# Performance work log

Measured on AMD Instinct MI355X. Metric: run time of the kernel, lower is better.

Reference implementation:

```python
import jax, jax.numpy as jnp
import numpy as np

B, S, A = 4096, 512, 64  # batch, state_dim, n_actions
H1, H2 = 1024, 512       # hidden_dims
EPS = 1e-8


def setup_inputs() -> dict:
    key = jax.random.key(0)
    ks = jax.random.split(key, 7)
    return {
        "states": jax.random.normal(ks[0], (B, S), dtype=jnp.float32),
        "W1": jax.random.normal(ks[1], (H1, S + A), dtype=jnp.float32) * 0.05,
        "b1": jax.random.normal(ks[2], (H1,), dtype=jnp.float32) * 0.01,
        "W2": jax.random.normal(ks[3], (H2, H1), dtype=jnp.float32) * 0.05,
        "b2": jax.random.normal(ks[4], (H2,), dtype=jnp.float32) * 0.01,
        "Wq": jax.random.normal(ks[5], (1, H2), dtype=jnp.float32) * 0.05,
        "bq": jax.random.normal(ks[6], (1,), dtype=jnp.float32) * 0.01,
    }


def _ff_layer(h, W, b):
    # L2-normalize over feature dim (torch dim=1 for 2D input), then linear + ReLU
    hn = h / (jnp.linalg.norm(h, axis=-1, keepdims=True) + EPS)
    return jax.nn.relu(jnp.einsum("abi,oi->abo", hn, W) + b)


def reference(states, W1, b1, W2, b2, Wq, bq):
    # Vectorized form of q_values: loop over actions becomes a leading axis a.
    # x_in[a, b] = concat(states[b], one_hot(a))  (overlay_type='standard')
    onehot = jnp.eye(A, dtype=states.dtype)                         # [A, A]
    x = jnp.concatenate(
        [jnp.broadcast_to(states[None], (A, B, S)),
         jnp.broadcast_to(onehot[:, None, :], (A, B, A))], axis=-1)  # [A, B, S+A]
    h = _ff_layer(x, W1, b1)   # [A, B, H1]
    h = _ff_layer(h, W2, b2)   # [A, B, H2]
    q = jnp.einsum("abh,oh->abo", h, Wq)[..., 0] + bq[0]            # [A, B]
    return q.T                                                       # [B, A]
```

## Files before the change

### kernel.cpp

```cpp
#include <hip/hip_runtime.h>
#include <stdint.h>

#define NB 4096
#define NS 512
#define NA 64
#define NH1 1024
#define NH2 512

typedef __attribute__((ext_vector_type(8))) short bf16x8;
typedef __attribute__((ext_vector_type(4))) float f32x4;

__device__ __forceinline__ unsigned short f2bf(float f) {
    union { float f; unsigned u; } v; v.f = f;
    return (unsigned short)((v.u + 0x8000u) >> 16);
}
__device__ __forceinline__ float bf2f(unsigned short h) {
    union { float f; unsigned u; } v; v.u = ((unsigned)h) << 16;
    return v.f;
}
__device__ __forceinline__ float bflo(unsigned u) {
    union { unsigned u; float f; } v; v.u = u << 16; return v.f;
}
__device__ __forceinline__ float bfhi(unsigned u) {
    union { unsigned u; float f; } v; v.u = u & 0xFFFF0000u; return v.f;
}
__device__ __forceinline__ unsigned packtrunc(float lo, float hi) {
    union { float f; unsigned u; } a, b; a.f = lo; b.f = hi;
    return __builtin_amdgcn_perm(b.u, a.u, 0x07060302u);
}
__device__ __forceinline__ void split2(float x, unsigned short& h, unsigned short& l) {
    unsigned short hh = f2bf(x);
    h = hh;
    l = f2bf(x - bf2f(hh));
}

__global__ void knorm(const float* __restrict__ S, float* __restrict__ nb) {
    int b = blockIdx.x; int l = threadIdx.x;
    const float* row = S + b * NS;
    float s = 0.f;
    for (int k = l; k < NS; k += 64) { float v = row[k]; s = fmaf(v, v, s); }
    for (int off = 32; off; off >>= 1) s += __shfl_down(s, off, 64);
    if (l == 0) nb[b] = sqrtf(s + 1.0f) + 1e-8f;
}

__global__ void kprep(const float* __restrict__ W1, const float* __restrict__ W2,
                      unsigned short* __restrict__ W2f, unsigned short* __restrict__ caT2) {
    int i = blockIdx.x * 256 + threadIdx.x;
    if (i < 524288) {
        int j = i & 7; int l = (i >> 3) & 63; int c = (i >> 9) & 31; int kc = i >> 14;
        int n = c * 16 + (l >> 2);
        int g = (l & 3) ^ ((n >> 1) & 3);
        int k = kc * 32 + g * 8 + j;
        W2f[i] = f2bf(W2[(size_t)n * NH1 + k]);
    } else {
        int j2 = i - 524288;
        int kk = j2 & 31; int a_loc = (j2 >> 5) & 15;
        int kc = (j2 >> 9) & 31; int att = j2 >> 14;
        int o = kc * 32 + kk;
        caT2[j2] = f2bf(W1[(size_t)o * 576 + 512 + att * 16 + a_loc]);
    }
}

__global__ __launch_bounds__(256) void kgemm1(
        const float* __restrict__ Sm, const float* __restrict__ W1,
        const float* __restrict__ b1, const float* __restrict__ nb,
        unsigned short* __restrict__ Gt) {
    const int m0 = (blockIdx.x >> 4) * 64;
    const int n0 = (blockIdx.x & 15) * 64;
    __shared__ unsigned short Ah[64][40], Al[64][40], Bh[64][40], Bl[64][40];
    int t = threadIdx.x;
    int lane = t & 63, wave = t >> 6;
    int wr = wave >> 1, wc = wave & 1;
    int qd = lane >> 4, cl = lane & 15;
    int r = t >> 2, seg = t & 3;
    f32x4 acc[2][2] = {};

    for (int k0 = 0; k0 < 512; k0 += 32) {
        {
            const float4* as4 = (const float4*)(Sm + (size_t)(m0 + r) * NS + k0 + seg * 8);
            const float4* bs4 = (const float4*)(W1 + (size_t)(n0 + r) * 576 + k0 + seg * 8);
            unsigned* ah = (unsigned*)&Ah[r][seg * 8];
            unsigned* al = (unsigned*)&Al[r][seg * 8];
            unsigned* bh = (unsigned*)&Bh[r][seg * 8];
            unsigned* bl = (unsigned*)&Bl[r][seg * 8];
#pragma unroll
            for (int v = 0; v < 2; v++) {
                float4 fa = as4[v];
                unsigned short h0,h1,h2,h3,l0,l1,l2,l3;
                split2(fa.x,h0,l0); split2(fa.y,h1,l1); split2(fa.z,h2,l2); split2(fa.w,h3,l3);
                ah[v*2]   = (unsigned)h0 | ((unsigned)h1 << 16);
                ah[v*2+1] = (unsigned)h2 | ((unsigned)h3 << 16);
                al[v*2]   = (unsigned)l0 | ((unsigned)l1 << 16);
                al[v*2+1] = (unsigned)l2 | ((unsigned)l3 << 16);
                float4 fb = bs4[v];
                split2(fb.x,h0,l0); split2(fb.y,h1,l1); split2(fb.z,h2,l2); split2(fb.w,h3,l3);
                bh[v*2]   = (unsigned)h0 | ((unsigned)h1 << 16);
                bh[v*2+1] = (unsigned)h2 | ((unsigned)h3 << 16);
                bl[v*2]   = (unsigned)l0 | ((unsigned)l1 << 16);
                bl[v*2+1] = (unsigned)l2 | ((unsigned)l3 << 16);
            }
        }
        __syncthreads();
        bf16x8 a_h[2], a_l[2], b_h[2], b_l[2];
#pragma unroll
        for (int mt = 0; mt < 2; mt++) {
            a_h[mt] = *(const bf16x8*)&Ah[wr*32 + mt*16 + cl][qd*8];
            a_l[mt] = *(const bf16x8*)&Al[wr*32 + mt*16 + cl][qd*8];
        }
#pragma unroll
        for (int nt = 0; nt < 2; nt++) {
            b_h[nt] = *(const bf16x8*)&Bh[wc*32 + nt*16 + cl][qd*8];
            b_l[nt] = *(const bf16x8*)&Bl[wc*32 + nt*16 + cl][qd*8];
        }
#pragma unroll
        for (int mt = 0; mt < 2; mt++)
#pragma unroll
            for (int nt = 0; nt < 2; nt++) {
                acc[mt][nt] = __builtin_amdgcn_mfma_f32_16x16x32_bf16(a_h[mt], b_h[nt], acc[mt][nt], 0, 0, 0);
                acc[mt][nt] = __builtin_amdgcn_mfma_f32_16x16x32_bf16(a_h[mt], b_l[nt], acc[mt][nt], 0, 0, 0);
                acc[mt][nt] = __builtin_amdgcn_mfma_f32_16x16x32_bf16(a_l[mt], b_h[nt], acc[mt][nt], 0, 0, 0);
            }
        __syncthreads();
    }
#pragma unroll
    for (int mt = 0; mt < 2; mt++)
#pragma unroll
        for (int i = 0; i < 4; i++) {
            int m = m0 + wr*32 + mt*16 + qd*4 + i;
            float nbv = nb[m];
#pragma unroll
            for (int nt = 0; nt < 2; nt++) {
                int n = n0 + wc*32 + nt*16 + cl;
                float val = fmaf(b1[n], nbv, acc[mt][nt][i]);
                Gt[((size_t)(n >> 5) * NB + m) * 32 + (n & 31)] = f2bf(val);
            }
        }
}

__global__ __launch_bounds__(256, 2) void kmain(
        const unsigned short* __restrict__ Gt,
        const unsigned short* __restrict__ caT2,
        const unsigned short* __restrict__ W2f,
        const float* __restrict__ nb,
        const float* __restrict__ b2, const float* __restrict__ Wq,
        const float* __restrict__ bq, float* __restrict__ out) {
    int bid = blockIdx.x;
    int at = bid & 3;
    int bt = bid >> 2;

    __shared__ __align__(16) unsigned short As[8][64][40];
    __shared__ float invnh[64];
    __shared__ float qred[64][4];

    int t = threadIdx.x;
    int lane = t & 63, wc = t >> 6;
    int l15 = lane & 15, l4 = lane >> 4;

    int row = t >> 2, kd = t & 3;
    int ab = row >> 2, bb = row & 3;
    const unsigned short* gG = Gt + ((size_t)(bt * 4 + bb)) * 32 + kd * 8;
    const unsigned short* gC = caT2 + (size_t)at * 16384 + ab * 32 + kd * 8;

    float sq = 0.f;
    f32x4 acc[4][8] = {};
    bf16x8 g_v, c_v;

    auto agen = [&](int slot) {
        const unsigned* gd = (const unsigned*)&g_v;
        const unsigned* cd = (const unsigned*)&c_v;
        unsigned ow[4];
#pragma unroll
        for (int p = 0; p < 4; p++) {
            float u0 = fmaxf(bflo(gd[p]) + bflo(cd[p]), 0.f);
            float u1 = fmaxf(bfhi(gd[p]) + bfhi(cd[p]), 0.f);
            sq = fmaf(u0, u0, sq);
            sq = fmaf(u1, u1, sq);
            ow[p] = packtrunc(u0, u1);
        }
        *(bf16x8*)&As[slot][row][kd * 8] = *(bf16x8*)ow;
    };

    const int boff = (wc * 128 + l15) * 32 + ((l4 ^ ((l15 >> 1) & 3)) << 3);
    const unsigned short* gB = W2f + boff;

    bf16x8 bfrL[4], bfrH[4];

    g_v = *(const bf16x8*)gG;
    c_v = *(const bf16x8*)gC;
#pragma unroll
    for (int p = 0; p < 4; ++p) {
        agen(p);
        gG += (size_t)NB * 32;
        gC += 512;
        g_v = *(const bf16x8*)gG;
        c_v = *(const bf16x8*)gC;
    }
#pragma unroll
    for (int j = 0; j < 4; j++)
        bfrL[j] = *(const bf16x8*)(gB + j * 512);
#pragma unroll
    for (int j = 0; j < 4; j++)
        bfrH[j] = *(const bf16x8*)(gB + (4 + j) * 512);
    gB += 16384;

    for (int it = 0; it < 32; ++it) {
        if ((it & 3) == 0) {
            asm volatile("s_waitcnt lgkmcnt(0)" ::: "memory");
            __builtin_amdgcn_s_barrier();
            __builtin_amdgcn_sched_barrier(0);
        }
        int rs = it & 7;

        bf16x8 af[4];
#pragma unroll
        for (int mt = 0; mt < 4; mt++)
            af[mt] = *(const bf16x8*)&As[rs][mt * 16 + l15][l4 * 8];

        if (it < 28) agen((it + 4) & 7);
        if (it < 27) {
            gG += (size_t)NB * 32;
            gC += 512;
            g_v = *(const bf16x8*)gG;
            c_v = *(const bf16x8*)gC;
        }

        __builtin_amdgcn_s_setprio(1);
#pragma unroll
        for (int nt = 0; nt < 4; nt++)
#pragma unroll
            for (int mt = 0; mt < 4; mt++)
                acc[mt][nt] = __builtin_amdgcn_mfma_f32_16x16x32_bf16(af[mt], bfrL[nt], acc[mt][nt], 0, 0, 0);
        __builtin_amdgcn_s_setprio(0);

        if (it < 31) {
#pragma unroll
            for (int j = 0; j < 4; j++)
                bfrL[j] = *(const bf16x8*)(gB + j * 512);
        }

        __builtin_amdgcn_s_setprio(1);
#pragma unroll
        for (int nt = 0; nt < 4; nt++)
#pragma unroll
            for (int mt = 0; mt < 4; mt++)
                acc[mt][4 + nt] = __builtin_amdgcn_mfma_f32_16x16x32_bf16(af[mt], bfrH[nt], acc[mt][4 + nt], 0, 0, 0);
        __builtin_amdgcn_s_setprio(0);

        if (it < 31) {
#pragma unroll
            for (int j = 0; j < 4; j++)
                bfrH[j] = *(const bf16x8*)(gB + (4 + j) * 512);
            gB += 16384;
        }
    }

    sq += __shfl_xor(sq, 1, 64);
    sq += __shfl_xor(sq, 2, 64);
    if (kd == 0) invnh[row] = 1.0f / (sqrtf(sq) + 1e-8f * nb[bt * 4 + bb]);
    __syncthreads();

    float wqv[8], b2v[8];
#pragma unroll
    for (int nt = 0; nt < 8; nt++) {
        int o = wc * 128 + nt * 16 + l15;
        wqv[nt] = Wq[o]; b2v[nt] = b2[o];
    }
#pragma unroll
    for (int mt = 0; mt < 4; mt++) {
#pragma unroll
        for (int i = 0; i < 4; i++) {
            int R = mt * 16 + l4 * 4 + i;
            float inv = invnh[R];
            float qp = 0.f;
#pragma unroll
            for (int nt = 0; nt < 8; nt++) {
                float z = fmaf(acc[mt][nt][i], inv, b2v[nt]);
                z = fmaxf(z, 0.f);
                qp = fmaf(z, wqv[nt], qp);
            }
            qp += __shfl_xor(qp, 1, 64);
            qp += __shfl_xor(qp, 2, 64);
            qp += __shfl_xor(qp, 4, 64);
            qp += __shfl_xor(qp, 8, 64);
            if (l15 == 0) qred[R][wc] = qp;
        }
    }
    __syncthreads();
    if (t < 64) {
        float qv = qred[t][0] + qred[t][1] + qred[t][2] + qred[t][3] + bq[0];
        int aa = at * 16 + (t >> 2);
        int bo = bt * 4 + (t & 3);
        out[(size_t)bo * NA + aa] = qv;
    }
}

extern "C" void kernel_launch(void* const* d_in, const int* in_sizes, int n_in,
                              void* d_out, int out_size, void* d_ws, size_t ws_size,
                              hipStream_t stream) {
    const float* states = (const float*)d_in[0];
    const float* W1     = (const float*)d_in[1];
    const float* b1     = (const float*)d_in[2];
    const float* W2     = (const float*)d_in[3];
    const float* b2     = (const float*)d_in[4];
    const float* Wq     = (const float*)d_in[5];
    const float* bq     = (const float*)d_in[6];
    float* out = (float*)d_out;

    char* ws = (char*)d_ws;
    unsigned short* Gt   = (unsigned short*)ws;
    unsigned short* W2f  = (unsigned short*)(ws + (8u << 20));
    unsigned short* caT2 = (unsigned short*)(ws + (9u << 20));
    float*          nbp  = (float*)(ws + (9u << 20) + (128u << 10));

    knorm<<<NB, 64, 0, stream>>>(states, nbp);
    kprep<<<2304, 256, 0, stream>>>(W1, W2, W2f, caT2);
    kgemm1<<<1024, 256, 0, stream>>>(states, W1, b1, nbp, Gt);
    kmain<<<4096, 256, 0, stream>>>(Gt, caT2, W2f, nbp, b2, Wq, bq, out);
}
```

Before: 317.9 us.

## Switch main GEMM to 32x32x16 bf16 MFMA with matching fragment layouts

Result: slower. 376.6 us (+18.5%).

```diff
diff --git a/kernel.cpp b/kernel.cpp
--- a/kernel.cpp
+++ b/kernel.cpp
@@ -9,6 +9,7 @@
 
 typedef __attribute__((ext_vector_type(8))) short bf16x8;
 typedef __attribute__((ext_vector_type(4))) float f32x4;
+typedef __attribute__((ext_vector_type(16))) float f32x16;
 
 __device__ __forceinline__ unsigned short f2bf(float f) {
     union { float f; unsigned u; } v; v.f = f;
@@ -47,10 +48,10 @@
                       unsigned short* __restrict__ W2f, unsigned short* __restrict__ caT2) {
     int i = blockIdx.x * 256 + threadIdx.x;
     if (i < 524288) {
-        int j = i & 7; int l = (i >> 3) & 63; int c = (i >> 9) & 31; int kc = i >> 14;
-        int n = c * 16 + (l >> 2);
-        int g = (l & 3) ^ ((n >> 1) & 3);
-        int k = kc * 32 + g * 8 + j;
+        int j = i & 7; int l = (i >> 3) & 63; int u = i >> 9;
+        int c = u & 15; int ks = (u >> 4) & 1; int kc = u >> 5;
+        int n = c * 32 + (l & 31);
+        int k = kc * 32 + ks * 16 + (l >> 5) * 8 + j;
         W2f[i] = f2bf(W2[(size_t)n * NH1 + k]);
     } else {
         int j2 = i - 524288;
@@ -148,13 +149,13 @@
     int at = bid & 3;
     int bt = bid >> 2;
 
-    __shared__ __align__(16) unsigned short As[8][64][40];
+    __shared__ __align__(16) unsigned short Asf[8][2048];
     __shared__ float invnh[64];
     __shared__ float qred[64][4];
 
     int t = threadIdx.x;
     int lane = t & 63, wc = t >> 6;
-    int l15 = lane & 15, l4 = lane >> 4;
+    int l31 = lane & 31, hi = lane >> 5;
 
     int row = t >> 2, kd = t & 3;
     int ab = row >> 2, bb = row & 3;
@@ -162,8 +163,10 @@
     const unsigned short* gC = caT2 + (size_t)at * 16384 + ab * 32 + kd * 8;
 
     float sq = 0.f;
-    f32x4 acc[4][8] = {};
+    f32x16 acc[2][4] = {};
     bf16x8 g_v, c_v;
+
+    const int aw = (((row >> 5) * 2 + (kd >> 1)) * 64 + ((kd & 1) * 32 + (row & 31))) * 8;
 
     auto agen = [&](int slot) {
         const unsigned* gd = (const unsigned*)&g_v;
@@ -177,11 +180,10 @@
             sq = fmaf(u1, u1, sq);
             ow[p] = packtrunc(u0, u1);
         }
-        *(bf16x8*)&As[slot][row][kd * 8] = *(bf16x8*)ow;
+        *(bf16x8*)&Asf[slot][aw] = *(bf16x8*)ow;
     };
 
-    const int boff = (wc * 128 + l15) * 32 + ((l4 ^ ((l15 >> 1) & 3)) << 3);
-    const unsigned short* gB = W2f + boff;
+    const unsigned short* gB = W2f + wc * 2048 + lane * 8;
 
     bf16x8 bfrL[4], bfrH[4];
 
@@ -200,7 +202,7 @@
         bfrL[j] = *(const bf16x8*)(gB + j * 512);
 #pragma unroll
     for (int j = 0; j < 4; j++)
-        bfrH[j] = *(const bf16x8*)(gB + (4 + j) * 512);
+        bfrH[j] = *(const bf16x8*)(gB + 8192 + j * 512);
     gB += 16384;
 
     for (int it = 0; it < 32; ++it) {
@@ -211,10 +213,12 @@
         }
         int rs = it & 7;
 
-        bf16x8 af[4];
-#pragma unroll
-        for (int mt = 0; mt < 4; mt++)
-            af[mt] = *(const bf16x8*)&As[rs][mt * 16 + l15][l4 * 8];
+        bf16x8 afL[2], afH[2];
+        const unsigned short* ab2 = &Asf[rs][lane * 8];
+        afL[0] = *(const bf16x8*)(ab2);
+        afH[0] = *(const bf16x8*)(ab2 + 512);
+        afL[1] = *(const bf16x8*)(ab2 + 1024);
+        afH[1] = *(const bf16x8*)(ab2 + 1536);
 
         if (it < 28) agen((it + 4) & 7);
         if (it < 27) {
@@ -228,8 +232,8 @@
 #pragma unroll
         for (int nt = 0; nt < 4; nt++)
 #pragma unroll
-            for (int mt = 0; mt < 4; mt++)
-                acc[mt][nt] = __builtin_amdgcn_mfma_f32_16x16x32_bf16(af[mt], bfrL[nt], acc[mt][nt], 0, 0, 0);
+            for (int mt = 0; mt < 2; mt++)
+                acc[mt][nt] = __builtin_amdgcn_mfma_f32_32x32x16_bf16(afL[mt], bfrL[nt], acc[mt][nt], 0, 0, 0);
         __builtin_amdgcn_s_setprio(0);
 
         if (it < 31) {
@@ -242,14 +246,14 @@
 #pragma unroll
         for (int nt = 0; nt < 4; nt++)
 #pragma unroll
-            for (int mt = 0; mt < 4; mt++)
-                acc[mt][4 + nt] = __builtin_amdgcn_mfma_f32_16x16x32_bf16(af[mt], bfrH[nt], acc[mt][4 + nt], 0, 0, 0);
+            for (int mt = 0; mt < 2; mt++)
+                acc[mt][nt] = __builtin_amdgcn_mfma_f32_32x32x16_bf16(afH[mt], bfrH[nt], acc[mt][nt], 0, 0, 0);
         __builtin_amdgcn_s_setprio(0);
 
         if (it < 31) {
 #pragma unroll
             for (int j = 0; j < 4; j++)
-                bfrH[j] = *(const bf16x8*)(gB + (4 + j) * 512);
+                bfrH[j] = *(const bf16x8*)(gB + 8192 + j * 512);
             gB += 16384;
         }
     }
@@ -259,22 +263,22 @@
     if (kd == 0) invnh[row] = 1.0f / (sqrtf(sq) + 1e-8f * nb[bt * 4 + bb]);
     __syncthreads();
 
-    float wqv[8], b2v[8];
-#pragma unroll
-    for (int nt = 0; nt < 8; nt++) {
-        int o = wc * 128 + nt * 16 + l15;
+    float wqv[4], b2v[4];
+#pragma unroll
+    for (int nt = 0; nt < 4; nt++) {
+        int o = wc * 128 + nt * 32 + l31;
         wqv[nt] = Wq[o]; b2v[nt] = b2[o];
     }
 #pragma unroll
-    for (int mt = 0; mt < 4; mt++) {
-#pragma unroll
-        for (int i = 0; i < 4; i++) {
-            int R = mt * 16 + l4 * 4 + i;
+    for (int mt = 0; mt < 2; mt++) {
+#pragma unroll
+        for (int r = 0; r < 16; r++) {
+            int R = mt * 32 + (r & 3) + 8 * (r >> 2) + 4 * hi;
             float inv = invnh[R];
             float qp = 0.f;
 #pragma unroll
-            for (int nt = 0; nt < 8; nt++) {
-                float z = fmaf(acc[mt][nt][i], inv, b2v[nt]);
+            for (int nt = 0; nt < 4; nt++) {
+                float z = fmaf(acc[mt][nt][r], inv, b2v[nt]);
                 z = fmaxf(z, 0.f);
                 qp = fmaf(z, wqv[nt], qp);
             }
@@ -282,7 +286,8 @@
             qp += __shfl_xor(qp, 2, 64);
             qp += __shfl_xor(qp, 4, 64);
             qp += __shfl_xor(qp, 8, 64);
-            if (l15 == 0) qred[R][wc] = qp;
+            qp += __shfl_xor(qp, 16, 64);
+            if (l31 == 0) qred[R][wc] = qp;
         }
     }
     __syncthreads();
```
